# Performance work log

Measured on AMD Instinct MI355X. Metric: run time of the kernel, lower is better.

## Reference

```python
import jax, jax.numpy as jnp
import numpy as np
from jax import lax

T, B, CIN, H, W = 16, 8, 16, 64, 64
HID = (32, 32)
K = 3


def _conv(x, w):
    # x: [B, C, H, W], w: [O, I, K, K], SAME padding, stride 1
    return lax.conv_general_dilated(
        x, w, window_strides=(1, 1), padding='SAME',
        dimension_numbers=('NCHW', 'OIHW', 'NCHW'))


def _run_layer(x_seq, w, b):
    # x_seq: [T, B, Cin_l, H, W]; w: [4*hid, Cin_l+hid, K, K]; b: [4*hid]
    hid = w.shape[0] // 4
    bsz = x_seq.shape[1]
    h0 = jnp.zeros((bsz, hid, H, W), x_seq.dtype)
    c0 = jnp.zeros_like(h0)

    def step(carry, xt):
        h, c = carry
        gates = _conv(jnp.concatenate([xt, h], axis=1), w) + b[None, :, None, None]
        i, f, o, g = jnp.split(gates, 4, axis=1)
        c_new = jax.nn.sigmoid(f) * c + jax.nn.sigmoid(i) * jnp.tanh(g)
        h_new = jax.nn.sigmoid(o) * jnp.tanh(c_new)
        return (h_new, c_new), h_new

    (h_T, c_T), h_seq = lax.scan(step, (h0, c0), x_seq)
    return h_seq, h_T, c_T


def setup_inputs() -> dict:
    key = jax.random.key(0)
    ks = jax.random.split(key, 5)
    x = jax.random.normal(ks[0], (T, B, CIN, H, W), dtype=jnp.float32)
    s0 = 1.0 / np.sqrt((CIN + HID[0]) * K * K)
    s1 = 1.0 / np.sqrt((HID[0] + HID[1]) * K * K)
    W0 = jax.random.normal(ks[1], (4 * HID[0], CIN + HID[0], K, K), dtype=jnp.float32) * s0
    b0 = jax.random.normal(ks[2], (4 * HID[0],), dtype=jnp.float32) * s0
    W1 = jax.random.normal(ks[3], (4 * HID[1], HID[0] + HID[1], K, K), dtype=jnp.float32) * s1
    b1 = jax.random.normal(ks[4], (4 * HID[1],), dtype=jnp.float32) * s1
    return {"x": x, "W0": W0, "b0": b0, "W1": W1, "b1": b1}


def reference(x, W0, b0, W1, b1):
    h_seq0, h0_T, c0_T = _run_layer(x, W0, b0)
    h_seq1, h1_T, c1_T = _run_layer(h_seq0, W1, b1)
    # return_all_layers=True: per-layer hidden sequences + per-layer final (h, c)
    return (h_seq0, h_seq1, h0_T, c0_T, h1_T, c1_T)
```

## Files before the change

### kernel.cpp

```cpp
#include <hip/hip_runtime.h>
#include <math.h>

#define TT   16
#define BATCH 8
#define HH   64
#define WW   64
#define HWSZ 4096
#define HID  32
#define CT_STRIDE 68

typedef __bf16 bf16x8 __attribute__((ext_vector_type(8)));
typedef float  f32x4  __attribute__((ext_vector_type(4)));
typedef unsigned short u16;
typedef unsigned int   u32;
typedef unsigned long long u64;
typedef u32 u32x4 __attribute__((ext_vector_type(4)));

__device__ __forceinline__ u16 f2bf(float f) {
    union { float f; u32 u; } v; v.f = f;
    u32 r = v.u + 0x7FFF + ((v.u >> 16) & 1);
    return (u16)(r >> 16);
}

__global__ __launch_bounds__(256)
void prep_x(const float* __restrict__ x, u16* __restrict__ xbf) {
    const int p = blockIdx.x * 256 + threadIdx.x;
    const int tb = p >> 12, pix = p & 4095;
    const float* src = x + ((size_t)tb * 16) * HWSZ + pix;
    u16 o[16];
#pragma unroll
    for (int c = 0; c < 16; ++c) o[c] = f2bf(src[(size_t)c * HWSZ]);
    uint4* dst = (uint4*)(xbf + (size_t)p * 16);
    dst[0] = *(uint4*)&o[0];
    dst[1] = *(uint4*)&o[8];
}

__global__ __launch_bounds__(256)
void prep_w(const float* __restrict__ W, u16* __restrict__ wf, int cinl) {
    const int idx = blockIdx.x * 256 + threadIdx.x;
    const int lane = idx & 63, nt = (idx >> 6) & 7, kc = (idx >> 9) & 1, tap = idx >> 10;
    const int cho = nt * 16 + (lane & 15);
    const int cb  = kc * 32 + ((lane >> 4) * 8);
    u16 o[8];
#pragma unroll
    for (int j = 0; j < 8; ++j) {
        const int cin = cb + j;
        o[j] = (cin < cinl) ? f2bf(W[((size_t)cho * cinl + cin) * 9 + tap]) : (u16)0;
    }
    ((uint4*)wf)[idx] = *(uint4*)&o[0];
}

__device__ __forceinline__ void conv_step(
    const u16* __restrict__ srcX, int xch,
    const u16* __restrict__ srcH,
    const uint4* __restrict__ wf,
    const float* __restrict__ bias,
    float* __restrict__ cbuf,
    float* __restrict__ hout, float* __restrict__ hT,
    u16* __restrict__ hbfo,
    int t0, int blk, uint4* lds4, float* ctile)
{
    const int tid = threadIdx.x;
    const int y0 = (blk & 31) * 2;
    const int b  = blk >> 5;

    for (int q = tid; q < 2112; q += 256) {
        const int c8 = q & 7;
        const int pr = q >> 3;
        const int px = pr % 66;
        const int r  = pr / 66;
        const int gy = y0 - 1 + r;
        const int gx = px - 1;
        uint4 v = {0u, 0u, 0u, 0u};
        if (gy >= 0 && gy < HH && gx >= 0 && gx < WW) {
            const int pix = b * HWSZ + gy * WW + gx;
            const int cin8 = c8 * 8;
            if (cin8 < xch) {
                v = *(const uint4*)(srcX + (size_t)pix * xch + cin8);
            } else if (cin8 < xch + 32) {
                if (!t0) v = *(const uint4*)(srcH + (size_t)pix * 32 + (cin8 - xch));
            }
        }
        lds4[(pr * 8 + c8) ^ (px & 7)] = v;
    }

    const int fr  = tid >> 2;
    const int fyy = fr >> 5, fc = fr & 31;
    const size_t gflat = ((size_t)(b * HID + fc) * HH + (y0 + fyy)) * WW;
    if (!t0) {
#pragma unroll
        for (int j = 0; j < 4; ++j) {
            const int q = j * 4 + (tid & 3);
            *(uint4*)(ctile + fr * CT_STRIDE + q * 4) =
                *(const uint4*)(cbuf + gflat + q * 4);
        }
    }
    __syncthreads();

    const int lane  = tid & 63;
    const int w     = tid >> 6;
    const int l15   = lane & 15, lhi = lane >> 4;
    const int khalf = w & 1;
    const int wrow  = w >> 1;

    float bv[4];
#pragma unroll
    for (int n = 0; n < 4; ++n) bv[n] = bias[n * 32 + khalf * 16 + l15];
    f32x4 acc[4][4];
#pragma unroll
    for (int m = 0; m < 4; ++m)
#pragma unroll
        for (int n = 0; n < 4; ++n)
            acc[m][n] = (f32x4){bv[n], bv[n], bv[n], bv[n]};

    const int p0 = l15 + 1;

    auto LOADA = [&](bf16x8* dst, int g) {
        const int tap = g >> 1, kc = g & 1;
        const int sr = wrow + tap / 3;
        const int dx = tap % 3 - 1;
        const int kcell = kc * 4 + lhi;
#pragma unroll
        for (int m = 0; m < 4; ++m) {
            const int pxt = p0 + m * 16 + dx;
            dst[m] = __builtin_bit_cast(bf16x8,
                     lds4[(((sr * 66 + pxt) * 8) + kcell) ^ (pxt & 7)]);
        }
    };
    auto LOADB = [&](bf16x8* dst, int g) {
#pragma unroll
        for (int n = 0; n < 4; ++n)
            dst[n] = __builtin_bit_cast(bf16x8,
                     wf[((size_t)g * 8 + (khalf + 2 * n)) * 64 + lane]);
    };
    auto MFMAG = [&](const bf16x8* a, const bf16x8* bw) {
#pragma unroll
        for (int n = 0; n < 4; ++n)
#pragma unroll
            for (int m = 0; m < 4; ++m)
                acc[m][n] = __builtin_amdgcn_mfma_f32_16x16x32_bf16(
                                a[m], bw[n], acc[m][n], 0, 0, 0);
    };

    bf16x8 a0[4], a1[4], a2[4], b0[4], b1[4], b2[4];
    LOADA(a0, 0); LOADB(b0, 0);
    LOADA(a1, 1); LOADB(b1, 1);
    LOADA(a2, 2); LOADB(b2, 2);
#pragma unroll
    for (int g = 0; g < 18; g += 3) {
        MFMAG(a0, b0);
        if (g + 3 < 18) { LOADA(a0, g + 3); LOADB(b0, g + 3); }
        MFMAG(a1, b1);
        if (g + 4 < 18) { LOADA(a1, g + 4); LOADB(b1, g + 4); }
        MFMAG(a2, b2);
        if (g + 5 < 18) { LOADA(a2, g + 5); LOADB(b2, g + 5); }
    }

    __syncthreads();
    float* htile = (float*)lds4;

    const int c = khalf * 16 + l15;
    const int row = wrow * 32 + c;
#pragma unroll
    for (int m = 0; m < 4; ++m) {
#pragma unroll
        for (int rr = 0; rr < 4; ++rr) {
            const int p = m * 16 + lhi * 4 + rr;
            const float cp = t0 ? 0.f : ctile[row * CT_STRIDE + p];
            const float iv = acc[m][0][rr], fv = acc[m][1][rr];
            const float ov = acc[m][2][rr], gv = acc[m][3][rr];
            const float ig = __builtin_amdgcn_rcpf(1.f + __expf(-iv));
            const float fg = __builtin_amdgcn_rcpf(1.f + __expf(-fv));
            const float og = __builtin_amdgcn_rcpf(1.f + __expf(-ov));
            const float gg = 1.f - 2.f * __builtin_amdgcn_rcpf(1.f + __expf(2.f * gv));
            const float cn = fg * cp + ig * gg;
            const float hn = og * (1.f - 2.f * __builtin_amdgcn_rcpf(1.f + __expf(2.f * cn)));
            ctile[row * CT_STRIDE + p] = cn;
            htile[row * CT_STRIDE + p] = hn;
        }
    }
    __syncthreads();

#pragma unroll
    for (int j = 0; j < 4; ++j) {
        const int q = j * 4 + (tid & 3);
        const u32x4 hv = *(const u32x4*)(htile + fr * CT_STRIDE + q * 4);
        const uint4 cv = *(const uint4*)(ctile + fr * CT_STRIDE + q * 4);
        __builtin_nontemporal_store(hv, (u32x4*)(hout + gflat + q * 4));
        *(uint4*)(cbuf + gflat + q * 4) = cv;
        if (hT) __builtin_nontemporal_store(hv, (u32x4*)(hT + gflat + q * 4));
    }

#pragma unroll
    for (int j = 0; j < 4; ++j) {
        const int idx = j * 256 + tid;
        const int c4  = idx & 7;
        const int pxx = (idx >> 3) & 63;
        const int yy  = idx >> 9;
        u16 pk[4];
#pragma unroll
        for (int k = 0; k < 4; ++k)
            pk[k] = f2bf(htile[(yy * 32 + c4 * 4 + k) * CT_STRIDE + pxx]);
        const int pix = b * HWSZ + (y0 + yy) * WW + pxx;
        *(u64*)(hbfo + (size_t)pix * 32 + c4 * 4) = *(u64*)pk;
    }
}

__global__ __launch_bounds__(256, 2)
void fused_step(
    const u16* srcX0, const u16* srcH0, const uint4* wf0, const float* bias0,
    float* cbuf0, float* hout0, float* hT0, u16* hbfo0, int t00, int act0,
    const u16* srcX1, const u16* srcH1, const uint4* wf1, const float* bias1,
    float* cbuf1, float* hout1, float* hT1, u16* hbfo1, int t01, int act1)
{
    __shared__ uint4 lds4[2112];
    __shared__ float ctile[64 * CT_STRIDE];
    const int blk = blockIdx.x;
    if (blk < 256) {
        if (!act0) return;
        conv_step(srcX0, 16, srcH0, wf0, bias0, cbuf0, hout0, hT0, hbfo0, t00, blk, lds4, ctile);
    } else {
        if (!act1) return;
        conv_step(srcX1, 32, srcH1, wf1, bias1, cbuf1, hout1, hT1, hbfo1, t01, blk - 256, lds4, ctile);
    }
}

extern "C" void kernel_launch(void* const* d_in, const int* in_sizes, int n_in,
                              void* d_out, int out_size, void* d_ws, size_t ws_size,
                              hipStream_t stream) {
    const float* x  = (const float*)d_in[0];
    const float* W0 = (const float*)d_in[1];
    const float* b0 = (const float*)d_in[2];
    const float* W1 = (const float*)d_in[3];
    const float* b1 = (const float*)d_in[4];
    float* out = (float*)d_out;

    float* hseq0 = out;
    float* hseq1 = out + 16777216;
    float* h0T   = out + 33554432;
    float* c0T   = out + 34603008;
    float* h1T   = out + 35651584;
    float* c1T   = out + 36700160;

    char* ws = (char*)d_ws;
    u16*  xbf = (u16*)ws;
    u16*  wf0 = (u16*)(ws + 16777216);
    u16*  wf1 = (u16*)(ws + 16777216 + 147456);
    u16*  hbf0[2] = { (u16*)(ws + 17072128), (u16*)(ws + 17072128 + 2097152) };
    u16*  hbf1[2] = { (u16*)(ws + 21266432), (u16*)(ws + 21266432 + 2097152) };

    prep_x<<<2048, 256, 0, stream>>>(x, xbf);
    prep_w<<<36, 256, 0, stream>>>(W0, wf0, 48);
    prep_w<<<36, 256, 0, stream>>>(W1, wf1, 64);

    const size_t hstep = (size_t)BATCH * HID * HWSZ;
    const size_t xstep = (size_t)BATCH * HWSZ * 16;

    for (int d = 0; d <= TT; ++d) {
        const int t0 = (d < TT) ? d : TT - 1;
        const int t1 = (d >= 1) ? d - 1 : 0;
        const int act0 = (d < TT), act1 = (d >= 1);
        fused_step<<<512, 256, 0, stream>>>(
            xbf + (size_t)t0 * xstep, hbf0[(t0 - 1) & 1],
            (const uint4*)wf0, b0, c0T,
            hseq0 + (size_t)t0 * hstep, (t0 == TT - 1 && act0) ? h0T : nullptr,
            hbf0[t0 & 1], (t0 == 0) ? 1 : 0, act0,
            hbf0[t1 & 1], hbf1[(t1 - 1) & 1],
            (const uint4*)wf1, b1, c1T,
            hseq1 + (size_t)t1 * hstep, (t1 == TT - 1 && act1) ? h1T : nullptr,
            hbf1[t1 & 1], (t1 == 0) ? 1 : 0, act1);
    }
}
```

Measured before the change: 300.8 us.

## Switch ConvLSTM gates to 32x32x16 MFMA and trim layer-0 K padding

Replaces the 16x16x32 bf16 MFMA tiling with 32x32x16 tiles. Gates are exchanged between half-waves via lane shuffles so each lane still gets all four gates for its pixel. The K dimension is now templated, so layer 0 uses 48 input channels in 3 chunks instead of padding to 64, which removes wasted MFMAs and LDS loads. The three prep kernels are merged into one launch. The trade-offs are added shuffle and select work in the epilogue and a new weight packing layout that must match the lane mapping.

```diff
diff --git a/kernel.cpp b/kernel.cpp
--- a/kernel.cpp
+++ b/kernel.cpp
@@ -10,7 +10,7 @@
 #define CT_STRIDE 68
 
 typedef __bf16 bf16x8 __attribute__((ext_vector_type(8)));
-typedef float  f32x4  __attribute__((ext_vector_type(4)));
+typedef float  f32x16 __attribute__((ext_vector_type(16)));
 typedef unsigned short u16;
 typedef unsigned int   u32;
 typedef unsigned long long u64;
@@ -22,25 +22,14 @@
     return (u16)(r >> 16);
 }
 
-__global__ __launch_bounds__(256)
-void prep_x(const float* __restrict__ x, u16* __restrict__ xbf) {
-    const int p = blockIdx.x * 256 + threadIdx.x;
-    const int tb = p >> 12, pix = p & 4095;
-    const float* src = x + ((size_t)tb * 16) * HWSZ + pix;
-    u16 o[16];
-#pragma unroll
-    for (int c = 0; c < 16; ++c) o[c] = f2bf(src[(size_t)c * HWSZ]);
-    uint4* dst = (uint4*)(xbf + (size_t)p * 16);
-    dst[0] = *(uint4*)&o[0];
-    dst[1] = *(uint4*)&o[8];
-}
-
-__global__ __launch_bounds__(256)
-void prep_w(const float* __restrict__ W, u16* __restrict__ wf, int cinl) {
-    const int idx = blockIdx.x * 256 + threadIdx.x;
-    const int lane = idx & 63, nt = (idx >> 6) & 7, kc = (idx >> 9) & 1, tap = idx >> 10;
-    const int cho = nt * 16 + (lane & 15);
-    const int cb  = kc * 32 + ((lane >> 4) * 8);
+__device__ __forceinline__ void prep_w32(const float* __restrict__ W,
+                                         u16* __restrict__ wf, int cinl, int idx) {
+    const int lane = idx & 63, T = (idx >> 6) & 3, kc16 = (idx >> 8) & 3, tap = idx >> 10;
+    const int col  = lane & 31;
+    const int gate = (T & 1) * 2 + (col >> 4);
+    const int hid  = (T >> 1) * 16 + (col & 15);
+    const int cho  = gate * HID + hid;
+    const int cb   = kc16 * 16 + (lane >> 5) * 8;
     u16 o[8];
 #pragma unroll
     for (int j = 0; j < 8; ++j) {
@@ -50,8 +39,31 @@
     ((uint4*)wf)[idx] = *(uint4*)&o[0];
 }
 
+__global__ __launch_bounds__(256)
+void prep_all(const float* __restrict__ x, u16* __restrict__ xbf,
+              const float* __restrict__ W0, u16* __restrict__ wf0,
+              const float* __restrict__ W1, u16* __restrict__ wf1) {
+    const int bid = blockIdx.x, tid = threadIdx.x;
+    if (bid < 2048) {
+        const int p = bid * 256 + tid;
+        const int tb = p >> 12, pix = p & 4095;
+        const float* src = x + ((size_t)tb * 16) * HWSZ + pix;
+        u16 o[16];
+#pragma unroll
+        for (int c = 0; c < 16; ++c) o[c] = f2bf(src[(size_t)c * HWSZ]);
+        uint4* dst = (uint4*)(xbf + (size_t)p * 16);
+        dst[0] = *(uint4*)&o[0];
+        dst[1] = *(uint4*)&o[8];
+    } else if (bid < 2084) {
+        prep_w32(W0, wf0, 48, (bid - 2048) * 256 + tid);
+    } else {
+        prep_w32(W1, wf1, 64, (bid - 2084) * 256 + tid);
+    }
+}
+
+template<int NKC, int XCH>
 __device__ __forceinline__ void conv_step(
-    const u16* __restrict__ srcX, int xch,
+    const u16* __restrict__ srcX,
     const u16* __restrict__ srcH,
     const uint4* __restrict__ wf,
     const float* __restrict__ bias,
@@ -60,13 +72,16 @@
     u16* __restrict__ hbfo,
     int t0, int blk, uint4* lds4, float* ctile)
 {
+    constexpr int NCH = (XCH + 32) / 8;
+    constexpr int NG  = 9 * NKC;
+
     const int tid = threadIdx.x;
     const int y0 = (blk & 31) * 2;
     const int b  = blk >> 5;
 
-    for (int q = tid; q < 2112; q += 256) {
-        const int c8 = q & 7;
-        const int pr = q >> 3;
+    for (int q = tid; q < 264 * NCH; q += 256) {
+        const int c8 = q % NCH;
+        const int pr = q / NCH;
         const int px = pr % 66;
         const int r  = pr / 66;
         const int gy = y0 - 1 + r;
@@ -75,10 +90,10 @@
         if (gy >= 0 && gy < HH && gx >= 0 && gx < WW) {
             const int pix = b * HWSZ + gy * WW + gx;
             const int cin8 = c8 * 8;
-            if (cin8 < xch) {
-                v = *(const uint4*)(srcX + (size_t)pix * xch + cin8);
-            } else if (cin8 < xch + 32) {
-                if (!t0) v = *(const uint4*)(srcH + (size_t)pix * 32 + (cin8 - xch));
+            if (cin8 < XCH) {
+                v = *(const uint4*)(srcX + (size_t)pix * XCH + cin8);
+            } else {
+                if (!t0) v = *(const uint4*)(srcH + (size_t)pix * 32 + (cin8 - XCH));
             }
         }
         lds4[(pr * 8 + c8) ^ (px & 7)] = v;
@@ -99,85 +114,94 @@
 
     const int lane  = tid & 63;
     const int w     = tid >> 6;
-    const int l15   = lane & 15, lhi = lane >> 4;
+    const int l31   = lane & 31, khi = lane >> 5;
+    const int l15   = lane & 15;
+    const int p     = l31 >> 4;
     const int khalf = w & 1;
     const int wrow  = w >> 1;
 
-    float bv[4];
-#pragma unroll
-    for (int n = 0; n < 4; ++n) bv[n] = bias[n * 32 + khalf * 16 + l15];
-    f32x4 acc[4][4];
-#pragma unroll
-    for (int m = 0; m < 4; ++m)
-#pragma unroll
-        for (int n = 0; n < 4; ++n)
-            acc[m][n] = (f32x4){bv[n], bv[n], bv[n], bv[n]};
-
-    const int p0 = l15 + 1;
+    float bv[2];
+#pragma unroll
+    for (int n = 0; n < 2; ++n)
+        bv[n] = bias[(2 * n + p) * HID + khalf * 16 + l15];
+
+    f32x16 acc[2][2];
+#pragma unroll
+    for (int m = 0; m < 2; ++m)
+#pragma unroll
+        for (int n = 0; n < 2; ++n)
+#pragma unroll
+            for (int j = 0; j < 16; ++j) acc[m][n][j] = bv[n];
 
     auto LOADA = [&](bf16x8* dst, int g) {
-        const int tap = g >> 1, kc = g & 1;
+        const int tap = g / NKC, kc = g % NKC;
         const int sr = wrow + tap / 3;
         const int dx = tap % 3 - 1;
-        const int kcell = kc * 4 + lhi;
-#pragma unroll
-        for (int m = 0; m < 4; ++m) {
-            const int pxt = p0 + m * 16 + dx;
+        const int c8 = kc * 2 + khi;
+#pragma unroll
+        for (int m = 0; m < 2; ++m) {
+            const int pxt = 1 + m * 32 + l31 + dx;
             dst[m] = __builtin_bit_cast(bf16x8,
-                     lds4[(((sr * 66 + pxt) * 8) + kcell) ^ (pxt & 7)]);
+                     lds4[(((sr * 66 + pxt) * 8) + c8) ^ (pxt & 7)]);
         }
     };
     auto LOADB = [&](bf16x8* dst, int g) {
-#pragma unroll
-        for (int n = 0; n < 4; ++n)
+        const int tap = g / NKC, kc = g % NKC;
+#pragma unroll
+        for (int n = 0; n < 2; ++n)
             dst[n] = __builtin_bit_cast(bf16x8,
-                     wf[((size_t)g * 8 + (khalf + 2 * n)) * 64 + lane]);
+                     wf[(((tap * 4 + kc) * 4) + (khalf * 2 + n)) * 64 + lane]);
     };
     auto MFMAG = [&](const bf16x8* a, const bf16x8* bw) {
 #pragma unroll
-        for (int n = 0; n < 4; ++n)
-#pragma unroll
-            for (int m = 0; m < 4; ++m)
-                acc[m][n] = __builtin_amdgcn_mfma_f32_16x16x32_bf16(
+        for (int n = 0; n < 2; ++n)
+#pragma unroll
+            for (int m = 0; m < 2; ++m)
+                acc[m][n] = __builtin_amdgcn_mfma_f32_32x32x16_bf16(
                                 a[m], bw[n], acc[m][n], 0, 0, 0);
     };
 
-    bf16x8 a0[4], a1[4], a2[4], b0[4], b1[4], b2[4];
+    bf16x8 a0[2], a1[2], a2[2], b0[2], b1[2], b2[2];
     LOADA(a0, 0); LOADB(b0, 0);
     LOADA(a1, 1); LOADB(b1, 1);
     LOADA(a2, 2); LOADB(b2, 2);
 #pragma unroll
-    for (int g = 0; g < 18; g += 3) {
+    for (int g = 0; g < NG; g += 3) {
         MFMAG(a0, b0);
-        if (g + 3 < 18) { LOADA(a0, g + 3); LOADB(b0, g + 3); }
+        if (g + 3 < NG) { LOADA(a0, g + 3); LOADB(b0, g + 3); }
         MFMAG(a1, b1);
-        if (g + 4 < 18) { LOADA(a1, g + 4); LOADB(b1, g + 4); }
+        if (g + 4 < NG) { LOADA(a1, g + 4); LOADB(b1, g + 4); }
         MFMAG(a2, b2);
-        if (g + 5 < 18) { LOADA(a2, g + 5); LOADB(b2, g + 5); }
+        if (g + 5 < NG) { LOADA(a2, g + 5); LOADB(b2, g + 5); }
     }
 
     __syncthreads();
     float* htile = (float*)lds4;
 
-    const int c = khalf * 16 + l15;
-    const int row = wrow * 32 + c;
-#pragma unroll
-    for (int m = 0; m < 4; ++m) {
-#pragma unroll
-        for (int rr = 0; rr < 4; ++rr) {
-            const int p = m * 16 + lhi * 4 + rr;
-            const float cp = t0 ? 0.f : ctile[row * CT_STRIDE + p];
-            const float iv = acc[m][0][rr], fv = acc[m][1][rr];
-            const float ov = acc[m][2][rr], gv = acc[m][3][rr];
-            const float ig = __builtin_amdgcn_rcpf(1.f + __expf(-iv));
-            const float fg = __builtin_amdgcn_rcpf(1.f + __expf(-fv));
-            const float og = __builtin_amdgcn_rcpf(1.f + __expf(-ov));
-            const float gg = 1.f - 2.f * __builtin_amdgcn_rcpf(1.f + __expf(2.f * gv));
-            const float cn = fg * cp + ig * gg;
-            const float hn = og * (1.f - 2.f * __builtin_amdgcn_rcpf(1.f + __expf(2.f * cn)));
-            ctile[row * CT_STRIDE + p] = cn;
-            htile[row * CT_STRIDE + p] = hn;
-        }
+    const int row = wrow * 32 + khalf * 16 + l15;
+#pragma unroll
+    for (int r = 0; r < 16; ++r) {
+        const float s0 = p ? acc[0][0][r] : acc[1][0][r];
+        const float s1 = p ? acc[0][1][r] : acc[1][1][r];
+        const float r0 = __shfl_xor(s0, 16);
+        const float r1 = __shfl_xor(s1, 16);
+        const float own0 = p ? acc[1][0][r] : acc[0][0][r];
+        const float own1 = p ? acc[1][1][r] : acc[0][1][r];
+        const float iv = p ? r0 : own0;
+        const float fv = p ? own0 : r0;
+        const float ov = p ? r1 : own1;
+        const float gv = p ? own1 : r1;
+        const int px = p * 32 + (r & 3) + 8 * (r >> 2) + 4 * khi;
+
+        const float cp = t0 ? 0.f : ctile[row * CT_STRIDE + px];
+        const float ig = __builtin_amdgcn_rcpf(1.f + __expf(-iv));
+        const float fg = __builtin_amdgcn_rcpf(1.f + __expf(-fv));
+        const float og = __builtin_amdgcn_rcpf(1.f + __expf(-ov));
+        const float gg = 1.f - 2.f * __builtin_amdgcn_rcpf(1.f + __expf(2.f * gv));
+        const float cn = fg * cp + ig * gg;
+        const float hn = og * (1.f - 2.f * __builtin_amdgcn_rcpf(1.f + __expf(2.f * cn)));
+        ctile[row * CT_STRIDE + px] = cn;
+        htile[row * CT_STRIDE + px] = hn;
     }
     __syncthreads();
 
@@ -218,10 +242,10 @@
     const int blk = blockIdx.x;
     if (blk < 256) {
         if (!act0) return;
-        conv_step(srcX0, 16, srcH0, wf0, bias0, cbuf0, hout0, hT0, hbfo0, t00, blk, lds4, ctile);
+        conv_step<3, 16>(srcX0, srcH0, wf0, bias0, cbuf0, hout0, hT0, hbfo0, t00, blk, lds4, ctile);
     } else {
         if (!act1) return;
-        conv_step(srcX1, 32, srcH1, wf1, bias1, cbuf1, hout1, hT1, hbfo1, t01, blk - 256, lds4, ctile);
+        conv_step<4, 32>(srcX1, srcH1, wf1, bias1, cbuf1, hout1, hT1, hbfo1, t01, blk - 256, lds4, ctile);
     }
 }
 
@@ -249,9 +273,7 @@
     u16*  hbf0[2] = { (u16*)(ws + 17072128), (u16*)(ws + 17072128 + 2097152) };
     u16*  hbf1[2] = { (u16*)(ws + 21266432), (u16*)(ws + 21266432 + 2097152) };
 
-    prep_x<<<2048, 256, 0, stream>>>(x, xbf);
-    prep_w<<<36, 256, 0, stream>>>(W0, wf0, 48);
-    prep_w<<<36, 256, 0, stream>>>(W1, wf1, 64);
+    prep_all<<<2120, 256, 0, stream>>>(x, xbf, W0, wf0, W1, wf1);
 
     const size_t hstep = (size_t)BATCH * HID * HWSZ;
     const size_t xstep = (size_t)BATCH * HWSZ * 16;
```

Measured after the change: 332.4 us. 10.5% more time.

## Enlarge conv tile to four rows per block and merge prep kernels

Applied to the files above, without the earlier changes.

Each block now computes four output rows instead of two, which halves the grid to 256 blocks and doubles the per-wave M accumulators to 8x4. Halo rows are shared by more outputs, so redundant LDS staging and weight loads are cut. The cell-state loads are issued into registers before the conv and written to LDS after it, to hide their latency. The three prep kernels are merged into one launch. In exchange, register pressure rises (launch bounds drop to 1 block per CU), prefetch depth falls from three stages to two, and only 256 blocks remain to fill the 256 CUs, so occupancy and latency hiding may suffer.

```diff
diff --git a/kernel.cpp b/kernel.cpp
--- a/kernel.cpp
+++ b/kernel.cpp
@@ -22,22 +22,8 @@
     return (u16)(r >> 16);
 }
 
-__global__ __launch_bounds__(256)
-void prep_x(const float* __restrict__ x, u16* __restrict__ xbf) {
-    const int p = blockIdx.x * 256 + threadIdx.x;
-    const int tb = p >> 12, pix = p & 4095;
-    const float* src = x + ((size_t)tb * 16) * HWSZ + pix;
-    u16 o[16];
-#pragma unroll
-    for (int c = 0; c < 16; ++c) o[c] = f2bf(src[(size_t)c * HWSZ]);
-    uint4* dst = (uint4*)(xbf + (size_t)p * 16);
-    dst[0] = *(uint4*)&o[0];
-    dst[1] = *(uint4*)&o[8];
-}
-
-__global__ __launch_bounds__(256)
-void prep_w(const float* __restrict__ W, u16* __restrict__ wf, int cinl) {
-    const int idx = blockIdx.x * 256 + threadIdx.x;
+__device__ __forceinline__ void prep_w16(const float* __restrict__ W,
+                                         u16* __restrict__ wf, int cinl, int idx) {
     const int lane = idx & 63, nt = (idx >> 6) & 7, kc = (idx >> 9) & 1, tap = idx >> 10;
     const int cho = nt * 16 + (lane & 15);
     const int cb  = kc * 32 + ((lane >> 4) * 8);
@@ -48,6 +34,28 @@
         o[j] = (cin < cinl) ? f2bf(W[((size_t)cho * cinl + cin) * 9 + tap]) : (u16)0;
     }
     ((uint4*)wf)[idx] = *(uint4*)&o[0];
+}
+
+__global__ __launch_bounds__(256)
+void prep_all(const float* __restrict__ x, u16* __restrict__ xbf,
+              const float* __restrict__ W0, u16* __restrict__ wf0,
+              const float* __restrict__ W1, u16* __restrict__ wf1) {
+    const int bid = blockIdx.x, tid = threadIdx.x;
+    if (bid < 2048) {
+        const int p = bid * 256 + tid;
+        const int tb = p >> 12, pix = p & 4095;
+        const float* src = x + ((size_t)tb * 16) * HWSZ + pix;
+        u16 o[16];
+#pragma unroll
+        for (int c = 0; c < 16; ++c) o[c] = f2bf(src[(size_t)c * HWSZ]);
+        uint4* dst = (uint4*)(xbf + (size_t)p * 16);
+        dst[0] = *(uint4*)&o[0];
+        dst[1] = *(uint4*)&o[8];
+    } else if (bid < 2084) {
+        prep_w16(W0, wf0, 48, (bid - 2048) * 256 + tid);
+    } else {
+        prep_w16(W1, wf1, 64, (bid - 2084) * 256 + tid);
+    }
 }
 
 __device__ __forceinline__ void conv_step(
@@ -61,10 +69,22 @@
     int t0, int blk, uint4* lds4, float* ctile)
 {
     const int tid = threadIdx.x;
-    const int y0 = (blk & 31) * 2;
-    const int b  = blk >> 5;
-
-    for (int q = tid; q < 2112; q += 256) {
+    const int y0 = (blk & 15) * 4;
+    const int b  = blk >> 4;
+
+    const int fr  = tid >> 1;
+    const int fyy = fr >> 5, fc = fr & 31;
+    const size_t gflat = ((size_t)(b * HID + fc) * HH + (y0 + fyy)) * WW;
+    uint4 cld[8];
+    if (!t0) {
+#pragma unroll
+        for (int j = 0; j < 8; ++j) {
+            const int q = j * 2 + (tid & 1);
+            cld[j] = *(const uint4*)(cbuf + gflat + q * 4);
+        }
+    }
+
+    for (int q = tid; q < 3168; q += 256) {
         const int c8 = q & 7;
         const int pr = q >> 3;
         const int px = pr % 66;
@@ -83,18 +103,6 @@
         }
         lds4[(pr * 8 + c8) ^ (px & 7)] = v;
     }
-
-    const int fr  = tid >> 2;
-    const int fyy = fr >> 5, fc = fr & 31;
-    const size_t gflat = ((size_t)(b * HID + fc) * HH + (y0 + fyy)) * WW;
-    if (!t0) {
-#pragma unroll
-        for (int j = 0; j < 4; ++j) {
-            const int q = j * 4 + (tid & 3);
-            *(uint4*)(ctile + fr * CT_STRIDE + q * 4) =
-                *(const uint4*)(cbuf + gflat + q * 4);
-        }
-    }
     __syncthreads();
 
     const int lane  = tid & 63;
@@ -106,9 +114,9 @@
     float bv[4];
 #pragma unroll
     for (int n = 0; n < 4; ++n) bv[n] = bias[n * 32 + khalf * 16 + l15];
-    f32x4 acc[4][4];
-#pragma unroll
-    for (int m = 0; m < 4; ++m)
+    f32x4 acc[8][4];
+#pragma unroll
+    for (int m = 0; m < 8; ++m)
 #pragma unroll
         for (int n = 0; n < 4; ++n)
             acc[m][n] = (f32x4){bv[n], bv[n], bv[n], bv[n]};
@@ -117,12 +125,12 @@
 
     auto LOADA = [&](bf16x8* dst, int g) {
         const int tap = g >> 1, kc = g & 1;
-        const int sr = wrow + tap / 3;
         const int dx = tap % 3 - 1;
         const int kcell = kc * 4 + lhi;
 #pragma unroll
-        for (int m = 0; m < 4; ++m) {
-            const int pxt = p0 + m * 16 + dx;
+        for (int m = 0; m < 8; ++m) {
+            const int sr = wrow * 2 + (m >> 2) + tap / 3;
+            const int pxt = p0 + (m & 3) * 16 + dx;
             dst[m] = __builtin_bit_cast(bf16x8,
                      lds4[(((sr * 66 + pxt) * 8) + kcell) ^ (pxt & 7)]);
         }
@@ -137,35 +145,40 @@
 #pragma unroll
         for (int n = 0; n < 4; ++n)
 #pragma unroll
-            for (int m = 0; m < 4; ++m)
+            for (int m = 0; m < 8; ++m)
                 acc[m][n] = __builtin_amdgcn_mfma_f32_16x16x32_bf16(
                                 a[m], bw[n], acc[m][n], 0, 0, 0);
     };
 
-    bf16x8 a0[4], a1[4], a2[4], b0[4], b1[4], b2[4];
+    bf16x8 a0[8], a1[8], b0[4], b1[4];
     LOADA(a0, 0); LOADB(b0, 0);
     LOADA(a1, 1); LOADB(b1, 1);
-    LOADA(a2, 2); LOADB(b2, 2);
-#pragma unroll
-    for (int g = 0; g < 18; g += 3) {
+#pragma unroll
+    for (int g = 0; g < 18; g += 2) {
         MFMAG(a0, b0);
-        if (g + 3 < 18) { LOADA(a0, g + 3); LOADB(b0, g + 3); }
+        if (g + 2 < 18) { LOADA(a0, g + 2); LOADB(b0, g + 2); }
         MFMAG(a1, b1);
-        if (g + 4 < 18) { LOADA(a1, g + 4); LOADB(b1, g + 4); }
-        MFMAG(a2, b2);
-        if (g + 5 < 18) { LOADA(a2, g + 5); LOADB(b2, g + 5); }
-    }
-
+        if (g + 3 < 18) { LOADA(a1, g + 3); LOADB(b1, g + 3); }
+    }
+
+    if (!t0) {
+#pragma unroll
+        for (int j = 0; j < 8; ++j) {
+            const int q = j * 2 + (tid & 1);
+            *(uint4*)(ctile + fr * CT_STRIDE + q * 4) = cld[j];
+        }
+    }
     __syncthreads();
+
     float* htile = (float*)lds4;
 
     const int c = khalf * 16 + l15;
-    const int row = wrow * 32 + c;
-#pragma unroll
-    for (int m = 0; m < 4; ++m) {
+#pragma unroll
+    for (int m = 0; m < 8; ++m) {
+        const int row = (wrow * 2 + (m >> 2)) * 32 + c;
 #pragma unroll
         for (int rr = 0; rr < 4; ++rr) {
-            const int p = m * 16 + lhi * 4 + rr;
+            const int p = (m & 3) * 16 + lhi * 4 + rr;
             const float cp = t0 ? 0.f : ctile[row * CT_STRIDE + p];
             const float iv = acc[m][0][rr], fv = acc[m][1][rr];
             const float ov = acc[m][2][rr], gv = acc[m][3][rr];
@@ -182,8 +195,8 @@
     __syncthreads();
 
 #pragma unroll
-    for (int j = 0; j < 4; ++j) {
-        const int q = j * 4 + (tid & 3);
+    for (int j = 0; j < 8; ++j) {
+        const int q = j * 2 + (tid & 1);
         const u32x4 hv = *(const u32x4*)(htile + fr * CT_STRIDE + q * 4);
         const uint4 cv = *(const uint4*)(ctile + fr * CT_STRIDE + q * 4);
         __builtin_nontemporal_store(hv, (u32x4*)(hout + gflat + q * 4));
@@ -192,7 +205,7 @@
     }
 
 #pragma unroll
-    for (int j = 0; j < 4; ++j) {
+    for (int j = 0; j < 8; ++j) {
         const int idx = j * 256 + tid;
         const int c4  = idx & 7;
         const int pxx = (idx >> 3) & 63;
@@ -206,22 +219,22 @@
     }
 }
 
-__global__ __launch_bounds__(256, 2)
+__global__ __launch_bounds__(256, 1)
 void fused_step(
     const u16* srcX0, const u16* srcH0, const uint4* wf0, const float* bias0,
     float* cbuf0, float* hout0, float* hT0, u16* hbfo0, int t00, int act0,
     const u16* srcX1, const u16* srcH1, const uint4* wf1, const float* bias1,
     float* cbuf1, float* hout1, float* hT1, u16* hbfo1, int t01, int act1)
 {
-    __shared__ uint4 lds4[2112];
-    __shared__ float ctile[64 * CT_STRIDE];
+    __shared__ uint4 lds4[3168];
+    __shared__ float ctile[128 * CT_STRIDE];
     const int blk = blockIdx.x;
-    if (blk < 256) {
+    if (blk < 128) {
         if (!act0) return;
         conv_step(srcX0, 16, srcH0, wf0, bias0, cbuf0, hout0, hT0, hbfo0, t00, blk, lds4, ctile);
     } else {
         if (!act1) return;
-        conv_step(srcX1, 32, srcH1, wf1, bias1, cbuf1, hout1, hT1, hbfo1, t01, blk - 256, lds4, ctile);
+        conv_step(srcX1, 32, srcH1, wf1, bias1, cbuf1, hout1, hT1, hbfo1, t01, blk - 128, lds4, ctile);
     }
 }
 
@@ -249,9 +262,7 @@
     u16*  hbf0[2] = { (u16*)(ws + 17072128), (u16*)(ws + 17072128 + 2097152) };
     u16*  hbf1[2] = { (u16*)(ws + 21266432), (u16*)(ws + 21266432 + 2097152) };
 
-    prep_x<<<2048, 256, 0, stream>>>(x, xbf);
-    prep_w<<<36, 256, 0, stream>>>(W0, wf0, 48);
-    prep_w<<<36, 256, 0, stream>>>(W1, wf1, 64);
+    prep_all<<<2120, 256, 0, stream>>>(x, xbf, W0, wf0, W1, wf1);
 
     const size_t hstep = (size_t)BATCH * HID * HWSZ;
     const size_t xstep = (size_t)BATCH * HWSZ * 16;
@@ -260,7 +271,7 @@
         const int t0 = (d < TT) ? d : TT - 1;
         const int t1 = (d >= 1) ? d - 1 : 0;
         const int act0 = (d < TT), act1 = (d >= 1);
-        fused_step<<<512, 256, 0, stream>>>(
+        fused_step<<<256, 256, 0, stream>>>(
             xbf + (size_t)t0 * xstep, hbf0[(t0 - 1) & 1],
             (const uint4*)wf0, b0, c0T,
             hseq0 + (size_t)t0 * hstep, (t0 == TT - 1 && act0) ? h0T : nullptr,
```

New measurement: 589.8 us. 96.1% more time.

## Load conv halo via direct global-to-LDS loads, swizzle ctile, fuse prep kernels

Applied to the files above, without the earlier changes.

The halo/input tile staging now uses global_load_lds to copy 16-byte chunks straight into LDS, with a zero page in workspace serving out-of-bounds and t=0 hidden-state reads. This removes the register round-trip and the branches. The c/h tile indexing gains an XOR swizzle to reduce LDS bank conflicts, MFMA blocks are bracketed with s_setprio, and the three prep kernels are merged into one launch plus a small memset. The direct LDS load relies on a lane-contiguous destination layout and on the zero-page trick, which adds a memset and some risk of mis-ordered swizzle.

```diff
diff --git a/kernel.cpp b/kernel.cpp
--- a/kernel.cpp
+++ b/kernel.cpp
@@ -22,22 +22,18 @@
     return (u16)(r >> 16);
 }
 
-__global__ __launch_bounds__(256)
-void prep_x(const float* __restrict__ x, u16* __restrict__ xbf) {
-    const int p = blockIdx.x * 256 + threadIdx.x;
-    const int tb = p >> 12, pix = p & 4095;
-    const float* src = x + ((size_t)tb * 16) * HWSZ + pix;
-    u16 o[16];
-#pragma unroll
-    for (int c = 0; c < 16; ++c) o[c] = f2bf(src[(size_t)c * HWSZ]);
-    uint4* dst = (uint4*)(xbf + (size_t)p * 16);
-    dst[0] = *(uint4*)&o[0];
-    dst[1] = *(uint4*)&o[8];
-}
-
-__global__ __launch_bounds__(256)
-void prep_w(const float* __restrict__ W, u16* __restrict__ wf, int cinl) {
-    const int idx = blockIdx.x * 256 + threadIdx.x;
+__device__ __forceinline__ int cidx(int row, int p) {
+    return row * CT_STRIDE + (p ^ ((row & 3) << 2));
+}
+
+__device__ __forceinline__ void gl2lds(const void* g, void* l) {
+    __builtin_amdgcn_global_load_lds(
+        (const __attribute__((address_space(1))) u32*)g,
+        (__attribute__((address_space(3))) u32*)l, 16, 0, 0);
+}
+
+__device__ __forceinline__ void prep_w16(const float* __restrict__ W,
+                                         u16* __restrict__ wf, int cinl, int idx) {
     const int lane = idx & 63, nt = (idx >> 6) & 7, kc = (idx >> 9) & 1, tap = idx >> 10;
     const int cho = nt * 16 + (lane & 15);
     const int cb  = kc * 32 + ((lane >> 4) * 8);
@@ -48,6 +44,28 @@
         o[j] = (cin < cinl) ? f2bf(W[((size_t)cho * cinl + cin) * 9 + tap]) : (u16)0;
     }
     ((uint4*)wf)[idx] = *(uint4*)&o[0];
+}
+
+__global__ __launch_bounds__(256)
+void prep_all(const float* __restrict__ x, u16* __restrict__ xbf,
+              const float* __restrict__ W0, u16* __restrict__ wf0,
+              const float* __restrict__ W1, u16* __restrict__ wf1) {
+    const int bid = blockIdx.x, tid = threadIdx.x;
+    if (bid < 2048) {
+        const int p = bid * 256 + tid;
+        const int tb = p >> 12, pix = p & 4095;
+        const float* src = x + ((size_t)tb * 16) * HWSZ + pix;
+        u16 o[16];
+#pragma unroll
+        for (int c = 0; c < 16; ++c) o[c] = f2bf(src[(size_t)c * HWSZ]);
+        uint4* dst = (uint4*)(xbf + (size_t)p * 16);
+        dst[0] = *(uint4*)&o[0];
+        dst[1] = *(uint4*)&o[8];
+    } else if (bid < 2084) {
+        prep_w16(W0, wf0, 48, (bid - 2048) * 256 + tid);
+    } else {
+        prep_w16(W1, wf1, 64, (bid - 2084) * 256 + tid);
+    }
 }
 
 __device__ __forceinline__ void conv_step(
@@ -57,31 +75,32 @@
     const float* __restrict__ bias,
     float* __restrict__ cbuf,
     float* __restrict__ hout, float* __restrict__ hT,
-    u16* __restrict__ hbfo,
+    u16* __restrict__ hbfo, const u16* __restrict__ zp,
     int t0, int blk, uint4* lds4, float* ctile)
 {
     const int tid = threadIdx.x;
     const int y0 = (blk & 31) * 2;
     const int b  = blk >> 5;
-
-    for (int q = tid; q < 2112; q += 256) {
-        const int c8 = q & 7;
+    const int lane = tid & 63;
+    const int w    = tid >> 6;
+
+    for (int j = w; j < 33; j += 4) {
+        const int q  = j * 64 + lane;
         const int pr = q >> 3;
         const int px = pr % 66;
         const int r  = pr / 66;
+        const int c8log = (q & 7) ^ (px & 7);
         const int gy = y0 - 1 + r;
         const int gx = px - 1;
-        uint4 v = {0u, 0u, 0u, 0u};
-        if (gy >= 0 && gy < HH && gx >= 0 && gx < WW) {
-            const int pix = b * HWSZ + gy * WW + gx;
-            const int cin8 = c8 * 8;
-            if (cin8 < xch) {
-                v = *(const uint4*)(srcX + (size_t)pix * xch + cin8);
-            } else if (cin8 < xch + 32) {
-                if (!t0) v = *(const uint4*)(srcH + (size_t)pix * 32 + (cin8 - xch));
-            }
-        }
-        lds4[(pr * 8 + c8) ^ (px & 7)] = v;
+        const int pix = b * HWSZ + gy * WW + gx;
+        const int cin8 = c8log * 8;
+        const bool inb = (gy >= 0) && (gy < HH) && (gx >= 0) && (gx < WW);
+        const u16* s =
+            (cin8 < xch) ? (srcX + (size_t)pix * xch + cin8)
+          : (cin8 < xch + 32) ? (t0 ? zp : (srcH + (size_t)pix * 32 + (cin8 - xch)))
+          : zp;
+        if (!inb) s = zp;
+        gl2lds(s, (void*)(lds4 + j * 64));
     }
 
     const int fr  = tid >> 2;
@@ -91,14 +110,12 @@
 #pragma unroll
         for (int j = 0; j < 4; ++j) {
             const int q = j * 4 + (tid & 3);
-            *(uint4*)(ctile + fr * CT_STRIDE + q * 4) =
+            *(uint4*)(ctile + cidx(fr, q * 4)) =
                 *(const uint4*)(cbuf + gflat + q * 4);
         }
     }
     __syncthreads();
 
-    const int lane  = tid & 63;
-    const int w     = tid >> 6;
     const int l15   = lane & 15, lhi = lane >> 4;
     const int khalf = w & 1;
     const int wrow  = w >> 1;
@@ -134,12 +151,14 @@
                      wf[((size_t)g * 8 + (khalf + 2 * n)) * 64 + lane]);
     };
     auto MFMAG = [&](const bf16x8* a, const bf16x8* bw) {
+        __builtin_amdgcn_s_setprio(1);
 #pragma unroll
         for (int n = 0; n < 4; ++n)
 #pragma unroll
             for (int m = 0; m < 4; ++m)
                 acc[m][n] = __builtin_amdgcn_mfma_f32_16x16x32_bf16(
                                 a[m], bw[n], acc[m][n], 0, 0, 0);
+        __builtin_amdgcn_s_setprio(0);
     };
 
     bf16x8 a0[4], a1[4], a2[4], b0[4], b1[4], b2[4];
@@ -166,7 +185,8 @@
 #pragma unroll
         for (int rr = 0; rr < 4; ++rr) {
             const int p = m * 16 + lhi * 4 + rr;
-            const float cp = t0 ? 0.f : ctile[row * CT_STRIDE + p];
+            const int ci = cidx(row, p);
+            const float cp = t0 ? 0.f : ctile[ci];
             const float iv = acc[m][0][rr], fv = acc[m][1][rr];
             const float ov = acc[m][2][rr], gv = acc[m][3][rr];
             const float ig = __builtin_amdgcn_rcpf(1.f + __expf(-iv));
@@ -175,8 +195,8 @@
             const float gg = 1.f - 2.f * __builtin_amdgcn_rcpf(1.f + __expf(2.f * gv));
             const float cn = fg * cp + ig * gg;
             const float hn = og * (1.f - 2.f * __builtin_amdgcn_rcpf(1.f + __expf(2.f * cn)));
-            ctile[row * CT_STRIDE + p] = cn;
-            htile[row * CT_STRIDE + p] = hn;
+            ctile[ci] = cn;
+            htile[ci] = hn;
         }
     }
     __syncthreads();
@@ -184,8 +204,9 @@
 #pragma unroll
     for (int j = 0; j < 4; ++j) {
         const int q = j * 4 + (tid & 3);
-        const u32x4 hv = *(const u32x4*)(htile + fr * CT_STRIDE + q * 4);
-        const uint4 cv = *(const uint4*)(ctile + fr * CT_STRIDE + q * 4);
+        const int ci = cidx(fr, q * 4);
+        const u32x4 hv = *(const u32x4*)(htile + ci);
+        const uint4 cv = *(const uint4*)(ctile + ci);
         __builtin_nontemporal_store(hv, (u32x4*)(hout + gflat + q * 4));
         *(uint4*)(cbuf + gflat + q * 4) = cv;
         if (hT) __builtin_nontemporal_store(hv, (u32x4*)(hT + gflat + q * 4));
@@ -200,7 +221,7 @@
         u16 pk[4];
 #pragma unroll
         for (int k = 0; k < 4; ++k)
-            pk[k] = f2bf(htile[(yy * 32 + c4 * 4 + k) * CT_STRIDE + pxx]);
+            pk[k] = f2bf(htile[cidx(yy * 32 + c4 * 4 + k, pxx)]);
         const int pix = b * HWSZ + (y0 + yy) * WW + pxx;
         *(u64*)(hbfo + (size_t)pix * 32 + c4 * 4) = *(u64*)pk;
     }
@@ -211,17 +232,18 @@
     const u16* srcX0, const u16* srcH0, const uint4* wf0, const float* bias0,
     float* cbuf0, float* hout0, float* hT0, u16* hbfo0, int t00, int act0,
     const u16* srcX1, const u16* srcH1, const uint4* wf1, const float* bias1,
-    float* cbuf1, float* hout1, float* hT1, u16* hbfo1, int t01, int act1)
+    float* cbuf1, float* hout1, float* hT1, u16* hbfo1, int t01, int act1,
+    const u16* zp)
 {
     __shared__ uint4 lds4[2112];
     __shared__ float ctile[64 * CT_STRIDE];
     const int blk = blockIdx.x;
     if (blk < 256) {
         if (!act0) return;
-        conv_step(srcX0, 16, srcH0, wf0, bias0, cbuf0, hout0, hT0, hbfo0, t00, blk, lds4, ctile);
+        conv_step(srcX0, 16, srcH0, wf0, bias0, cbuf0, hout0, hT0, hbfo0, zp, t00, blk, lds4, ctile);
     } else {
         if (!act1) return;
-        conv_step(srcX1, 32, srcH1, wf1, bias1, cbuf1, hout1, hT1, hbfo1, t01, blk - 256, lds4, ctile);
+        conv_step(srcX1, 32, srcH1, wf1, bias1, cbuf1, hout1, hT1, hbfo1, zp, t01, blk - 256, lds4, ctile);
     }
 }
 
@@ -248,10 +270,10 @@
     u16*  wf1 = (u16*)(ws + 16777216 + 147456);
     u16*  hbf0[2] = { (u16*)(ws + 17072128), (u16*)(ws + 17072128 + 2097152) };
     u16*  hbf1[2] = { (u16*)(ws + 21266432), (u16*)(ws + 21266432 + 2097152) };
-
-    prep_x<<<2048, 256, 0, stream>>>(x, xbf);
-    prep_w<<<36, 256, 0, stream>>>(W0, wf0, 48);
-    prep_w<<<36, 256, 0, stream>>>(W1, wf1, 64);
+    u16*  zp = (u16*)(ws + 25460736);
+
+    (void)hipMemsetAsync(zp, 0, 64, stream);
+    prep_all<<<2120, 256, 0, stream>>>(x, xbf, W0, wf0, W1, wf1);
 
     const size_t hstep = (size_t)BATCH * HID * HWSZ;
     const size_t xstep = (size_t)BATCH * HWSZ * 16;
@@ -268,6 +290,7 @@
             hbf0[t1 & 1], hbf1[(t1 - 1) & 1],
             (const uint4*)wf1, b1, c1T,
             hseq1 + (size_t)t1 * hstep, (t1 == TT - 1 && act1) ? h1T : nullptr,
-            hbf1[t1 & 1], (t1 == 0) ? 1 : 0, act1);
-    }
-}
+            hbf1[t1 & 1], (t1 == 0) ? 1 : 0, act1,
+            zp);
+    }
+}
```

After: 261.3 us. 1.15x faster.
